# Kernel optimization log

Measured on AMD Instinct MI355X. Metric: run time of the kernel, lower is better.

## Reference

```python
import jax, jax.numpy as jnp
import numpy as np

B, S, H, NH = 4, 2048, 512, 8
HD = H // NH  # head dim = 64


def setup_inputs() -> dict:
    key = jax.random.key(0)
    ks = jax.random.split(key, 12)
    f = lambda k, sh: jax.random.normal(k, sh, dtype=jnp.float32)
    w = lambda k: f(k, (H, H)) * 0.02  # Linear weight (out, in), torch-style
    return {
        "q": f(ks[0], (B, S, H)),
        "k": f(ks[1], (B, S, H)),
        "v": f(ks[2], (B, S, H)),
        "mask": jax.random.randint(ks[3], (B, S, S), 0, 2, dtype=jnp.int32),
        "Wq": w(ks[4]), "bq": jnp.zeros((H,), jnp.float32),
        "Wk": w(ks[5]), "bk": jnp.zeros((H,), jnp.float32),
        "Wv": w(ks[6]), "bv": jnp.zeros((H,), jnp.float32),
        "Wo": w(ks[7]), "bo": jnp.zeros((H,), jnp.float32),
    }


def reference(q, k, v, mask, Wq, bq, Wk, bk, Wv, bv, Wo, bo):
    b, s, h = q.shape
    scale = jnp.asarray(np.sqrt(HD), q.dtype)
    # QKV projections (torch Linear: x @ W.T + b), split into heads: b n s h
    def heads(x, W, bias):
        y = x @ W.T + bias
        return y.reshape(b, s, NH, HD).transpose(0, 2, 1, 3)
    Q = heads(q, Wq, bq)
    K = heads(k, Wk, bk)
    V = heads(v, Wv, bv)
    scores = jnp.einsum('bnsh,bnth->bnst', Q, K) / scale
    scores = jnp.where(mask[:, None, :, :] == 0, jnp.asarray(-1e9, scores.dtype), scores)
    attn = jax.nn.softmax(scores, axis=-1)
    # dropout is identity in eval mode
    out = jnp.einsum('bnst,bnth->bnsh', attn, V)
    out = out.transpose(0, 2, 1, 3).reshape(b, s, h)
    return out @ Wo.T + bo
```

## Files before the change

kernel.cpp:

```cpp
#include <hip/hip_runtime.h>
#include <cstdint>


typedef __bf16 bf16x8 __attribute__((ext_vector_type(8)));
typedef float  f32x4  __attribute__((ext_vector_type(4)));
typedef float  f32x16 __attribute__((ext_vector_type(16)));

#define MFMA16(a, b, c) __builtin_amdgcn_mfma_f32_16x16x32_bf16(a, b, c, 0, 0, 0)
#define MFMA32(a, b, c) __builtin_amdgcn_mfma_f32_32x32x16_bf16(a, b, c, 0, 0, 0)

__device__ __forceinline__ ushort f2bf(float f) {
  union { __bf16 h; ushort u; } v; v.h = (__bf16)f; return v.u;
}

typedef const __attribute__((address_space(1))) unsigned int* gas_u32;
typedef __attribute__((address_space(3))) unsigned int* las_u32;
__device__ __forceinline__ void gll16(const void* g, void* l) {
  __builtin_amdgcn_global_load_lds((gas_u32)g, (las_u32)l, 16, 0, 0);
}

__global__ __launch_bounds__(256) void cvt_w(
    const float* __restrict__ w0, const float* __restrict__ w1,
    const float* __restrict__ w2, const float* __restrict__ w3,
    ushort* __restrict__ dst) {
  const float* src = (blockIdx.y == 0) ? w0 : (blockIdx.y == 1) ? w1
                   : (blockIdx.y == 2) ? w2 : w3;
  ushort* d = dst + (size_t)blockIdx.y * 262144;
  int i = blockIdx.x * 256 + threadIdx.x;
  for (int j = i; j < 65536; j += 16384) {
    float4 v = ((const float4*)src)[j];
    ushort4 o = { f2bf(v.x), f2bf(v.y), f2bf(v.z), f2bf(v.w) };
    ((ushort4*)d)[j] = o;
  }
}

__global__ __launch_bounds__(256) void mask_bits_kernel(
    const int* __restrict__ mask, unsigned long long* __restrict__ MB) {
  const int lane = threadIdx.x & 63;
  const int wv = (int)((blockIdx.x * 256 + threadIdx.x) >> 6);
  const size_t base = (size_t)wv * 64;
  for (int j = 0; j < 64; j += 4) {
    int v0 = mask[(base + j + 0) * 64 + lane];
    int v1 = mask[(base + j + 1) * 64 + lane];
    int v2 = mask[(base + j + 2) * 64 + lane];
    int v3 = mask[(base + j + 3) * 64 + lane];
    unsigned long long b0 = __ballot(v0 != 0), b1 = __ballot(v1 != 0);
    unsigned long long b2 = __ballot(v2 != 0), b3 = __ballot(v3 != 0);
    if (lane == 0) {
      MB[base + j] = b0; MB[base + j + 1] = b1;
      MB[base + j + 2] = b2; MB[base + j + 3] = b3;
    }
  }
}

__global__ __launch_bounds__(256, 3) void qkv_gemm(
    const float* __restrict__ q, const float* __restrict__ k,
    const float* __restrict__ v, const ushort* __restrict__ Wb,
    const float* __restrict__ bq, const float* __restrict__ bk,
    const float* __restrict__ bv, ushort* __restrict__ Qh,
    ushort* __restrict__ Kh, ushort* __restrict__ Vt) {
  __shared__ float  Asf[128 * 64];
  __shared__ ushort Ws[128 * 64];
  const int z = blockIdx.z;
  const float* X = (z == 0) ? q : (z == 1) ? k : v;
  const ushort* W = Wb + (size_t)z * 262144;
  const float* bias = (z == 0) ? bq : (z == 1) ? bk : bv;
  const float scale = (z == 0) ? 0.18033688011112042f : 1.0f;
  ushort* Y = (z == 0) ? Qh : (z == 1) ? Kh : Vt;

  const int tid = threadIdx.x, wv = tid >> 6, l = tid & 63;
  const int quad = l >> 4, ln = l & 15;
  const int m0 = blockIdx.x * 128, n0 = blockIdx.y * 128;
  const int wm = (wv & 1) * 64, wn = (wv >> 1) * 64;
  const int srA = l >> 4, sA = l & 15, cA = sA >> 1, hA = sA & 1;
  const int srW = l >> 3, scW = l & 7;
  f32x4 acc[4][4] = {};

  for (int kk = 0; kk < 512; kk += 64) {
#pragma unroll
    for (int i = 0; i < 8; ++i) {
      int rowa = wv * 32 + i * 4 + srA;
      gll16(X + (size_t)(m0 + rowa) * 512 + kk + ((cA ^ (rowa & 7)) * 8 + hA * 4),
            Asf + (wv * 32 + i * 4) * 64);
    }
#pragma unroll
    for (int i = 0; i < 4; ++i) {
      int roww = wv * 32 + i * 8 + srW;
      gll16(W + (size_t)(n0 + roww) * 512 + kk + ((scW ^ (roww & 7)) * 8),
            Ws + (wv * 32 + i * 8) * 64);
    }
    __syncthreads();
#pragma unroll
    for (int ks = 0; ks < 2; ++ks) {
      bf16x8 a[4], bw[4];
#pragma unroll
      for (int mt = 0; mt < 4; ++mt) {
        int row = wm + mt * 16 + ln;
        int p = (ks * 4 + quad) ^ (row & 7);
        const float* ap = &Asf[row * 64 + p * 8];
        f32x4 x0 = *(const f32x4*)ap;
        f32x4 x1 = *(const f32x4*)(ap + 4);
        bf16x8 t;
#pragma unroll
        for (int j = 0; j < 4; ++j) { t[j] = (__bf16)x0[j]; t[4 + j] = (__bf16)x1[j]; }
        a[mt] = t;
      }
#pragma unroll
      for (int nt = 0; nt < 4; ++nt) {
        int row = wn + nt * 16 + ln;
        bw[nt] = *(const bf16x8*)&Ws[row * 64 + (((ks * 4 + quad) ^ (row & 7)) * 8)];
      }
#pragma unroll
      for (int mt = 0; mt < 4; ++mt)
#pragma unroll
        for (int nt = 0; nt < 4; ++nt)
          acc[mt][nt] = MFMA16(a[mt], bw[nt], acc[mt][nt]);
    }
    __syncthreads();
  }
  float bval[4];
#pragma unroll
  for (int nt = 0; nt < 4; ++nt) bval[nt] = bias[n0 + wn + nt * 16 + ln];

  if (z == 2) {
    ushort* uT = (ushort*)Asf;
#pragma unroll
    for (int nt = 0; nt < 4; ++nt) {
      int row = wn + nt * 16 + ln;
#pragma unroll
      for (int mt = 0; mt < 4; ++mt) {
        int mbase = wm + mt * 16 + quad * 4;
        ushort4 pk;
        pk.x = f2bf(acc[mt][nt][0] + bval[nt]);
        pk.y = f2bf(acc[mt][nt][1] + bval[nt]);
        pk.z = f2bf(acc[mt][nt][2] + bval[nt]);
        pk.w = f2bf(acc[mt][nt][3] + bval[nt]);
        int c = (mbase >> 3) ^ (row & 7);
        *(ushort4*)&uT[row * 128 + c * 8 + (quad & 1) * 4] = pk;
      }
    }
    __syncthreads();
#pragma unroll
    for (int j = 0; j < 8; ++j) {
      int i = tid + j * 256;
      int row = i >> 4, cs = i & 15;
      int g = cs ^ (row & 7);
      uint4 d = *(const uint4*)&uT[row * 128 + cs * 8];
      int n = n0 + row, m = m0 + g * 8;
      int bb = m >> 11, s = m & 2047, h = n >> 6, hd = n & 63;
      *(uint4*)(Y + ((size_t)((bb * 8 + h) * 64 + hd)) * 2048 + s) = d;
    }
  } else {
#pragma unroll
    for (int mt = 0; mt < 4; ++mt)
#pragma unroll
      for (int nt = 0; nt < 4; ++nt) {
        int n = n0 + wn + nt * 16 + ln;
#pragma unroll
        for (int r = 0; r < 4; ++r) {
          int m = m0 + wm + mt * 16 + quad * 4 + r;
          float val = (acc[mt][nt][r] + bval[nt]) * scale;
          int bb = m >> 11, s = m & 2047, h = n >> 6, hd = n & 63;
          Y[(((size_t)(bb * 8 + h) * 2048) + s) * 64 + hd] = f2bf(val);
        }
      }
  }
}

__global__ __launch_bounds__(256, 4) void attn(
    const ushort* __restrict__ Qh, const ushort* __restrict__ Kh,
    const ushort* __restrict__ Vt, const unsigned long long* __restrict__ MB,
    ushort* __restrict__ O) {
  __shared__ ushort SMEM[16384];
  ushort* Ks = SMEM;
  ushort* Vs = SMEM + 8192;
  const int tid = threadIdx.x, wv = tid >> 6, lane = tid & 63;
  const int hs = lane >> 5, lq = lane & 31;
  const int qh = wv >> 1, kvh = wv & 1;
  const int bh = blockIdx.x, qb = blockIdx.y;
  const size_t hoff = (size_t)bh * 2048 * 64;
  const int q0 = qb * 64;
  const int qg = q0 + qh * 32 + lq;
  const int srK = lane >> 3, scK = lane & 7;
  const int srV = lane >> 4, scV = lane & 15;

  bf16x8 qf[4];
#pragma unroll
  for (int ki = 0; ki < 4; ++ki)
    qf[ki] = *(const bf16x8*)(Qh + hoff + (size_t)qg * 64 + ki * 16 + hs * 8);

  f32x16 po0 = {}, po1 = {};
  float l_own = 0.f;
  const unsigned long long* mrow = MB + ((size_t)(bh >> 3) * 2048 + qg) * 32;

  for (int it = 0; it < 16; ++it) {
    const int kv0 = it * 128;
#pragma unroll
    for (int i = 0; i < 4; ++i) {
      int row = wv * 32 + i * 8 + srK;
      gll16(Kh + hoff + (size_t)(kv0 + row) * 64 + ((scK ^ (row & 7)) * 8),
            Ks + (wv * 32 + i * 8) * 64);
      int rv = wv * 16 + i * 4 + srV;
      gll16(Vt + hoff + (size_t)rv * 2048 + kv0 + ((scV ^ (rv & 7)) * 8),
            Vs + (wv * 16 + i * 4) * 128);
    }
    unsigned long long mbw = mrow[it * 2 + kvh];
    __syncthreads();

#pragma unroll
    for (int ch = 0; ch < 2; ++ch) {
      const int kvb = kvh * 64 + ch * 32;
      f32x16 sc_ = {};
#pragma unroll
      for (int ki = 0; ki < 4; ++ki) {
        int row = kvb + lq;
        bf16x8 ak = *(const bf16x8*)&Ks[row * 64 + (((2 * ki + hs) ^ (row & 7)) * 8)];
        sc_ = MFMA32(ak, qf[ki], sc_);
      }
      uint pk[8];
      float psum = 0.f;
#pragma unroll
      for (int c = 0; c < 4; ++c) {
        unsigned nib = (unsigned)(mbw >> (ch * 32 + c * 8 + hs * 4)) & 0xFu;
        float p0 = (nib & 1u) ? exp2f(sc_[4 * c + 0]) : 0.f;
        float p1 = (nib & 2u) ? exp2f(sc_[4 * c + 1]) : 0.f;
        float p2 = (nib & 4u) ? exp2f(sc_[4 * c + 2]) : 0.f;
        float p3 = (nib & 8u) ? exp2f(sc_[4 * c + 3]) : 0.f;
        psum += (p0 + p1) + (p2 + p3);
        pk[2 * c + 0] = (uint)f2bf(p0) | ((uint)f2bf(p1) << 16);
        pk[2 * c + 1] = (uint)f2bf(p2) | ((uint)f2bf(p3) << 16);
      }
      l_own += psum;
      uint bx[4];
#pragma unroll
      for (int t2 = 0; t2 < 2; ++t2)
#pragma unroll
        for (int b2 = 0; b2 < 2; ++b2) {
          uint snd = hs ? pk[4 * t2 + b2] : pk[4 * t2 + 2 + b2];
          bx[t2 * 2 + b2] = (uint)__shfl_xor((int)snd, 32);
        }
#pragma unroll
      for (int t2 = 0; t2 < 2; ++t2) {
        union { uint u[4]; bf16x8 v; } bp;
        bp.u[0] = hs ? bx[2 * t2 + 0] : pk[4 * t2 + 0];
        bp.u[1] = hs ? bx[2 * t2 + 1] : pk[4 * t2 + 1];
        bp.u[2] = hs ? pk[4 * t2 + 2] : bx[2 * t2 + 0];
        bp.u[3] = hs ? pk[4 * t2 + 3] : bx[2 * t2 + 1];
#pragma unroll
        for (int m2 = 0; m2 < 2; ++m2) {
          int hd = m2 * 32 + lq;
          int gch = (kvb >> 3) + 2 * t2 + hs;
          bf16x8 av = *(const bf16x8*)&Vs[hd * 128 + ((gch ^ (hd & 7)) * 8)];
          if (m2 == 0) po0 = MFMA32(av, bp.v, po0);
          else         po1 = MFMA32(av, bp.v, po1);
        }
      }
    }
    __syncthreads();
  }

  l_own += __shfl_xor(l_own, 32);
  float* psh = (float*)Ks;
  float* lsh = (float*)Vs;
  ushort* Osh = Vs + 256;
  if (kvh == 1) {
#pragma unroll
    for (int i = 0; i < 16; ++i) psh[(qh * 32 + i) * 64 + lane] = po0[i];
#pragma unroll
    for (int i = 0; i < 16; ++i) psh[(qh * 32 + 16 + i) * 64 + lane] = po1[i];
    lsh[qh * 64 + lane] = l_own;
  }
  __syncthreads();
  if (kvh == 0) {
    float linv = 1.0f / (l_own + lsh[qh * 64 + lane]);
    int row = qh * 32 + lq;
#pragma unroll
    for (int m2 = 0; m2 < 2; ++m2) {
#pragma unroll
      for (int c = 0; c < 4; ++c)
#pragma unroll
        for (int b2 = 0; b2 < 2; ++b2) {
          int r = 4 * c + 2 * b2;
          float v0, v1;
          if (m2 == 0) {
            v0 = (po0[r] + psh[(qh * 32 + r) * 64 + lane]) * linv;
            v1 = (po0[r + 1] + psh[(qh * 32 + r + 1) * 64 + lane]) * linv;
          } else {
            v0 = (po1[r] + psh[(qh * 32 + 16 + r) * 64 + lane]) * linv;
            v1 = (po1[r + 1] + psh[(qh * 32 + 16 + r + 1) * 64 + lane]) * linv;
          }
          int hd = m2 * 32 + 8 * c + 4 * hs + 2 * b2;
          *(uint*)&Osh[row * 72 + hd] = (uint)f2bf(v0) | ((uint)f2bf(v1) << 16);
        }
    }
  }
  __syncthreads();
  for (int i = tid; i < 512; i += 256) {
    int row = i >> 3, cc = i & 7;
    uint4 d = *(const uint4*)&Osh[row * 72 + cc * 8];
    *(uint4*)(O + ((size_t)((bh >> 3) * 2048 + q0 + row)) * 512 +
              (bh & 7) * 64 + cc * 8) = d;
  }
}

__global__ __launch_bounds__(256) void out_gemm(
    const ushort* __restrict__ X, const ushort* __restrict__ W,
    const float* __restrict__ bias, float* __restrict__ Y) {
  __shared__ ushort As[64 * 64];
  __shared__ ushort Ws[128 * 64];
  const int tid = threadIdx.x, wv = tid >> 6, l = tid & 63;
  const int quad = l >> 4, ln = l & 15;
  const int m0 = blockIdx.x * 64, n0 = blockIdx.y * 128;
  const int wm = (wv & 1) * 32, wn = (wv >> 1) * 64;
  const int sr = l >> 3, sc = l & 7;
  f32x4 acc[2][4] = {};
  for (int kk = 0; kk < 512; kk += 64) {
#pragma unroll
    for (int i = 0; i < 2; ++i) {
      int row = wv * 16 + i * 8 + sr;
      gll16(X + (size_t)(m0 + row) * 512 + kk + ((sc ^ (row & 7)) * 8),
            As + (wv * 16 + i * 8) * 64);
    }
#pragma unroll
    for (int i = 0; i < 4; ++i) {
      int row = wv * 32 + i * 8 + sr;
      gll16(W + (size_t)(n0 + row) * 512 + kk + ((sc ^ (row & 7)) * 8),
            Ws + (wv * 32 + i * 8) * 64);
    }
    __syncthreads();
#pragma unroll
    for (int ks = 0; ks < 2; ++ks) {
      bf16x8 a[2], bw[4];
#pragma unroll
      for (int mt = 0; mt < 2; ++mt) {
        int row = wm + mt * 16 + ln;
        a[mt] = *(const bf16x8*)&As[row * 64 + (((ks * 4 + quad) ^ (row & 7)) * 8)];
      }
#pragma unroll
      for (int nt = 0; nt < 4; ++nt) {
        int row = wn + nt * 16 + ln;
        bw[nt] = *(const bf16x8*)&Ws[row * 64 + (((ks * 4 + quad) ^ (row & 7)) * 8)];
      }
#pragma unroll
      for (int mt = 0; mt < 2; ++mt)
#pragma unroll
        for (int nt = 0; nt < 4; ++nt)
          acc[mt][nt] = MFMA16(a[mt], bw[nt], acc[mt][nt]);
    }
    __syncthreads();
  }
#pragma unroll
  for (int mt = 0; mt < 2; ++mt)
#pragma unroll
    for (int nt = 0; nt < 4; ++nt) {
      int n = n0 + wn + nt * 16 + ln;
      float bval = bias[n];
#pragma unroll
      for (int r = 0; r < 4; ++r) {
        int m = m0 + wm + mt * 16 + quad * 4 + r;
        Y[(size_t)m * 512 + n] = acc[mt][nt][r] + bval;
      }
    }
}

extern "C" void kernel_launch(void* const* d_in, const int* in_sizes, int n_in,
                              void* d_out, int out_size, void* d_ws, size_t ws_size,
                              hipStream_t stream) {
  const float* q    = (const float*)d_in[0];
  const float* k    = (const float*)d_in[1];
  const float* v    = (const float*)d_in[2];
  const int*   mask = (const int*)d_in[3];
  const float* Wq   = (const float*)d_in[4];
  const float* bq   = (const float*)d_in[5];
  const float* Wk   = (const float*)d_in[6];
  const float* bk   = (const float*)d_in[7];
  const float* Wv   = (const float*)d_in[8];
  const float* bv   = (const float*)d_in[9];
  const float* Wo   = (const float*)d_in[10];
  const float* bo   = (const float*)d_in[11];
  float* out = (float*)d_out;

  uint8_t* ws = (uint8_t*)d_ws;
  const size_t MiB = 1u << 20;
  ushort* Oh = (ushort*)(ws + 0 * MiB);
  ushort* Qh = (ushort*)(ws + 8 * MiB);
  ushort* Kh = (ushort*)(ws + 16 * MiB);
  ushort* Vt = (ushort*)(ws + 24 * MiB);
  unsigned long long* MB = (unsigned long long*)(ws + 32 * MiB);
  ushort* Wb = (ushort*)(ws + 34 * MiB);

  cvt_w<<<dim3(64, 4), 256, 0, stream>>>(Wq, Wk, Wv, Wo, Wb);
  mask_bits_kernel<<<1024, 256, 0, stream>>>(mask, MB);
  qkv_gemm<<<dim3(64, 4, 3), 256, 0, stream>>>(q, k, v, Wb, bq, bk, bv, Qh, Kh, Vt);
  attn<<<dim3(32, 32), 256, 0, stream>>>(Qh, Kh, Vt, MB, Oh);
  out_gemm<<<dim3(128, 4), 256, 0, stream>>>(Oh, Wb + 3 * 262144, bo, out);
}
```

Baseline: 268.5 us.

## Cheapen bf16 packing, use MFMA row-sum, stage Q/K stores through LDS

Replaces the compiler's bf16 conversion with round-half-up integer packing plus a byte-permute that packs two values at once. Uses the raw hardware exp2 builtin. Computes the softmax denominator with an extra MFMA against a ones vector instead of scalar adds and a cross-lane shuffle. Q/K projection outputs are now staged through padded shared memory so each thread writes 16-byte coalesced stores instead of scattered 2-byte ones. This adds one MFMA per P-tile and more shared-memory use in qkv_gemm, which may reduce occupancy. The rounding also differs slightly from round-to-nearest-even.

```diff
diff --git a/kernel.cpp b/kernel.cpp
--- a/kernel.cpp
+++ b/kernel.cpp
@@ -10,7 +10,23 @@
 #define MFMA32(a, b, c) __builtin_amdgcn_mfma_f32_32x32x16_bf16(a, b, c, 0, 0, 0)
 
 __device__ __forceinline__ ushort f2bf(float f) {
-  union { __bf16 h; ushort u; } v; v.h = (__bf16)f; return v.u;
+  union { float f; uint32_t u; } v; v.f = f;
+  return (ushort)((v.u + 0x8000u) >> 16);
+}
+__device__ __forceinline__ uint packbf(float a, float b) {
+  union { float f; uint32_t u; } x, y; x.f = a; y.f = b;
+#if __has_builtin(__builtin_amdgcn_perm)
+  return __builtin_amdgcn_perm(y.u + 0x8000u, x.u + 0x8000u, 0x07060302u);
+#else
+  return ((x.u + 0x8000u) >> 16) | ((y.u + 0x8000u) & 0xffff0000u);
+#endif
+}
+__device__ __forceinline__ float exp2r(float x) {
+#if __has_builtin(__builtin_amdgcn_exp2f)
+  return __builtin_amdgcn_exp2f(x);
+#else
+  return exp2f(x);
+#endif
 }
 
 typedef const __attribute__((address_space(1))) unsigned int* gas_u32;
@@ -29,8 +45,8 @@
   int i = blockIdx.x * 256 + threadIdx.x;
   for (int j = i; j < 65536; j += 16384) {
     float4 v = ((const float4*)src)[j];
-    ushort4 o = { f2bf(v.x), f2bf(v.y), f2bf(v.z), f2bf(v.w) };
-    ((ushort4*)d)[j] = o;
+    uint2 o = { packbf(v.x, v.y), packbf(v.z, v.w) };
+    ((uint2*)d)[j] = o;
   }
 }
 
@@ -59,8 +75,9 @@
     const float* __restrict__ bq, const float* __restrict__ bk,
     const float* __restrict__ bv, ushort* __restrict__ Qh,
     ushort* __restrict__ Kh, ushort* __restrict__ Vt) {
-  __shared__ float  Asf[128 * 64];
+  __shared__ ushort SH[128 * 136];
   __shared__ ushort Ws[128 * 64];
+  float* Asf = (float*)SH;
   const int z = blockIdx.z;
   const float* X = (z == 0) ? q : (z == 1) ? k : v;
   const ushort* W = Wb + (size_t)z * 262144;
@@ -100,10 +117,12 @@
         const float* ap = &Asf[row * 64 + p * 8];
         f32x4 x0 = *(const f32x4*)ap;
         f32x4 x1 = *(const f32x4*)(ap + 4);
-        bf16x8 t;
-#pragma unroll
-        for (int j = 0; j < 4; ++j) { t[j] = (__bf16)x0[j]; t[4 + j] = (__bf16)x1[j]; }
-        a[mt] = t;
+        union { uint u[4]; bf16x8 v; } t;
+        t.u[0] = packbf(x0[0], x0[1]);
+        t.u[1] = packbf(x0[2], x0[3]);
+        t.u[2] = packbf(x1[0], x1[1]);
+        t.u[3] = packbf(x1[2], x1[3]);
+        a[mt] = t.v;
       }
 #pragma unroll
       for (int nt = 0; nt < 4; ++nt) {
@@ -123,20 +142,17 @@
   for (int nt = 0; nt < 4; ++nt) bval[nt] = bias[n0 + wn + nt * 16 + ln];
 
   if (z == 2) {
-    ushort* uT = (ushort*)Asf;
+    ushort* uT = SH;
 #pragma unroll
     for (int nt = 0; nt < 4; ++nt) {
       int row = wn + nt * 16 + ln;
 #pragma unroll
       for (int mt = 0; mt < 4; ++mt) {
         int mbase = wm + mt * 16 + quad * 4;
-        ushort4 pk;
-        pk.x = f2bf(acc[mt][nt][0] + bval[nt]);
-        pk.y = f2bf(acc[mt][nt][1] + bval[nt]);
-        pk.z = f2bf(acc[mt][nt][2] + bval[nt]);
-        pk.w = f2bf(acc[mt][nt][3] + bval[nt]);
+        uint2 pk = { packbf(acc[mt][nt][0] + bval[nt], acc[mt][nt][1] + bval[nt]),
+                     packbf(acc[mt][nt][2] + bval[nt], acc[mt][nt][3] + bval[nt]) };
         int c = (mbase >> 3) ^ (row & 7);
-        *(ushort4*)&uT[row * 128 + c * 8 + (quad & 1) * 4] = pk;
+        *(uint2*)&uT[row * 128 + c * 8 + (quad & 1) * 4] = pk;
       }
     }
     __syncthreads();
@@ -151,19 +167,28 @@
       *(uint4*)(Y + ((size_t)((bb * 8 + h) * 64 + hd)) * 2048 + s) = d;
     }
   } else {
+    ushort* uM = SH;
 #pragma unroll
     for (int mt = 0; mt < 4; ++mt)
 #pragma unroll
       for (int nt = 0; nt < 4; ++nt) {
-        int n = n0 + wn + nt * 16 + ln;
+        int n = wn + nt * 16 + ln;
 #pragma unroll
         for (int r = 0; r < 4; ++r) {
-          int m = m0 + wm + mt * 16 + quad * 4 + r;
-          float val = (acc[mt][nt][r] + bval[nt]) * scale;
-          int bb = m >> 11, s = m & 2047, h = n >> 6, hd = n & 63;
-          Y[(((size_t)(bb * 8 + h) * 2048) + s) * 64 + hd] = f2bf(val);
+          int m = wm + mt * 16 + quad * 4 + r;
+          uM[m * 136 + n] = f2bf((acc[mt][nt][r] + bval[nt]) * scale);
         }
       }
+    __syncthreads();
+#pragma unroll
+    for (int j = 0; j < 8; ++j) {
+      int i = tid + j * 256;
+      int row = i >> 4, cs = i & 15;
+      uint4 d = *(const uint4*)&uM[row * 136 + cs * 8];
+      int m = m0 + row, n = n0 + cs * 8;
+      int bb = m >> 11, s = m & 2047, h = n >> 6, hd = n & 63;
+      *(uint4*)(Y + (((size_t)(bb * 8 + h) * 2048) + s) * 64 + hd) = d;
+    }
   }
 }
 
@@ -189,8 +214,12 @@
   for (int ki = 0; ki < 4; ++ki)
     qf[ki] = *(const bf16x8*)(Qh + hoff + (size_t)qg * 64 + ki * 16 + hs * 8);
 
+  bf16x8 ones;
+#pragma unroll
+  for (int j = 0; j < 8; ++j) ones[j] = (__bf16)1.0f;
+
   f32x16 po0 = {}, po1 = {};
-  float l_own = 0.f;
+  f32x16 lacc = {};
   const unsigned long long* mrow = MB + ((size_t)(bh >> 3) * 2048 + qg) * 32;
 
   for (int it = 0; it < 16; ++it) {
@@ -218,19 +247,16 @@
         sc_ = MFMA32(ak, qf[ki], sc_);
       }
       uint pk[8];
-      float psum = 0.f;
 #pragma unroll
       for (int c = 0; c < 4; ++c) {
         unsigned nib = (unsigned)(mbw >> (ch * 32 + c * 8 + hs * 4)) & 0xFu;
-        float p0 = (nib & 1u) ? exp2f(sc_[4 * c + 0]) : 0.f;
-        float p1 = (nib & 2u) ? exp2f(sc_[4 * c + 1]) : 0.f;
-        float p2 = (nib & 4u) ? exp2f(sc_[4 * c + 2]) : 0.f;
-        float p3 = (nib & 8u) ? exp2f(sc_[4 * c + 3]) : 0.f;
-        psum += (p0 + p1) + (p2 + p3);
-        pk[2 * c + 0] = (uint)f2bf(p0) | ((uint)f2bf(p1) << 16);
-        pk[2 * c + 1] = (uint)f2bf(p2) | ((uint)f2bf(p3) << 16);
-      }
-      l_own += psum;
+        float p0 = (nib & 1u) ? exp2r(sc_[4 * c + 0]) : 0.f;
+        float p1 = (nib & 2u) ? exp2r(sc_[4 * c + 1]) : 0.f;
+        float p2 = (nib & 4u) ? exp2r(sc_[4 * c + 2]) : 0.f;
+        float p3 = (nib & 8u) ? exp2r(sc_[4 * c + 3]) : 0.f;
+        pk[2 * c + 0] = packbf(p0, p1);
+        pk[2 * c + 1] = packbf(p2, p3);
+      }
       uint bx[4];
 #pragma unroll
       for (int t2 = 0; t2 < 2; ++t2)
@@ -246,6 +272,7 @@
         bp.u[1] = hs ? bx[2 * t2 + 1] : pk[4 * t2 + 1];
         bp.u[2] = hs ? pk[4 * t2 + 2] : bx[2 * t2 + 0];
         bp.u[3] = hs ? pk[4 * t2 + 3] : bx[2 * t2 + 1];
+        lacc = MFMA32(ones, bp.v, lacc);
 #pragma unroll
         for (int m2 = 0; m2 < 2; ++m2) {
           int hd = m2 * 32 + lq;
@@ -259,7 +286,7 @@
     __syncthreads();
   }
 
-  l_own += __shfl_xor(l_own, 32);
+  float l_own = lacc[0];
   float* psh = (float*)Ks;
   float* lsh = (float*)Vs;
   ushort* Osh = Vs + 256;
@@ -290,7 +317,7 @@
             v1 = (po1[r + 1] + psh[(qh * 32 + 16 + r + 1) * 64 + lane]) * linv;
           }
           int hd = m2 * 32 + 8 * c + 4 * hs + 2 * b2;
-          *(uint*)&Osh[row * 72 + hd] = (uint)f2bf(v0) | ((uint)f2bf(v1) << 16);
+          *(uint*)&Osh[row * 72 + hd] = packbf(v0, v1);
         }
     }
   }
```

Result: faster. 261.9 us (-2.5%).
